# Optimization experiments

Measured on AMD Instinct MI355X. Metric: run time of the kernel, lower is better.

The kernel has to match this reference:

```python
import jax, jax.numpy as jnp
import numpy as np

NX = 65536   # spatial cells
T = 32       # time points
H = 128      # MLP hidden width
DX = 1.0     # spatial resolution (init kwarg dx)
S0, S1 = -1.0, 1.0  # fixed stencil (learn_stencil=False)


def setup_inputs() -> dict:
    key = jax.random.key(0)
    k1, k2, k3, k4 = jax.random.split(key, 4)
    t = jnp.arange(T, dtype=jnp.float32) * 0.01          # time grid, dt=0.01
    u0 = jax.random.uniform(k1, (NX,), jnp.float32)      # initial state
    inv_sqrt_h = jnp.float32(1.0 / np.sqrt(H))
    W1 = jax.random.normal(k2, (1, H), jnp.float32)
    W2 = jax.random.normal(k3, (H, H), jnp.float32) * inv_sqrt_h
    W3 = jax.random.normal(k4, (H, 1), jnp.float32) * inv_sqrt_h
    D = jnp.full((1,), 0.01, jnp.float32)                # diffusion coefficient
    BC = jnp.zeros((2, 1), jnp.float32)                  # Dirichlet BC values
    return {"t": t, "u0": u0, "W1": W1, "W2": W2, "W3": W3, "D": D, "BC": BC}


def _flux(u, W1, W2, W3, D, BC):
    # per-cell MLP (func_nn): Linear->Tanh->Linear->Tanh->Linear, no bias, no sigmoid
    h = jnp.tanh(u[:, None] @ W1)        # [Nx, H]
    h = jnp.tanh(h @ W2)                 # [Nx, H]
    a = (h @ W3)[:, 0]                   # [Nx]
    a_plus = jax.nn.relu(a)
    a_min = -jax.nn.relu(-a)
    d = D[0]
    # left fluxes
    lb = d * (S0 * u[0] + S1 * BC[0, 0]) - a_plus[0] / DX * (-S0 * u[0] - S1 * BC[0, 0])
    ln = d * (S0 * u[1:] + S1 * u[:-1]) - a_plus[1:] / DX * (-S0 * u[1:] - S1 * u[:-1])
    left = jnp.concatenate([lb[None], ln])
    # right fluxes
    rb = d * (S0 * u[-1] + S1 * BC[1, 0]) - a_min[-1] / DX * (S0 * u[-1] + S1 * BC[1, 0])
    rn = d * (S0 * u[:-1] + S1 * u[1:]) - a_min[:-1] / DX * (S0 * u[:-1] + S1 * u[1:])
    right = jnp.concatenate([rn, rb[None]])
    return left + right


def reference(t, u0, W1, W2, W3, D, BC):
    # Neural-ODE integration of du/dt = flux_kernel(u); fixed-step RK4 over grid t
    f = lambda u: _flux(u, W1, W2, W3, D, BC)

    def step(u, dt):
        k1 = f(u)
        k2 = f(u + 0.5 * dt * k1)
        k3 = f(u + 0.5 * dt * k2)
        k4 = f(u + dt * k3)
        un = u + (dt / 6.0) * (k1 + 2.0 * k2 + 2.0 * k3 + k4)
        return un, un

    _, us = jax.lax.scan(step, u0, jnp.diff(t))
    return jnp.concatenate([u0[None], us], axis=0)  # [T, Nx]
```

## Files before the change

### kernel.cpp

```cpp
#include <hip/hip_runtime.h>

#define NXC 65536
#define TT 32
#define HH 128
#define TABN 6145
#define TABNP 6146
#define TABLO (-1.0f)
#define TABINV 2048.0f
#define OUTW 32
#define VC 2
#define WINW 128
#define HALO 48

typedef __attribute__((ext_vector_type(8))) short bf16x8;
typedef __attribute__((ext_vector_type(4))) float f32x4;
typedef unsigned short u16;

__device__ __forceinline__ float bf2f(u16 b) {
    union { unsigned int u; float f; } v; v.u = ((unsigned int)b) << 16; return v.f;
}
__device__ __forceinline__ u16 f2bf(float f) {
    union { float f; unsigned int u; } v; v.f = f;
    return (u16)((v.u + 0x7fffu + ((v.u >> 16) & 1u)) >> 16);
}
__device__ __forceinline__ bool is_bf16_mode(const void* t) {
    return ((const u16*)t)[1] != 0;
}

#if __has_builtin(__builtin_amdgcn_exp2f)
#define EXP2F(x) __builtin_amdgcn_exp2f(x)
#else
#define EXP2F(x) exp2f(x)
#endif
#if __has_builtin(__builtin_amdgcn_rcpf)
#define RCPF(x) __builtin_amdgcn_rcpf(x)
#else
#define RCPF(x) (1.0f / (x))
#endif

__device__ __forceinline__ float fast_tanh(float x) {
    float e = EXP2F(x * 2.8853900817779268f);
    return 1.0f - 2.0f * RCPF(e + 1.0f);
}

__global__ void w2swz_kernel(const void* t, const void* W2,
                             u16* __restrict__ w2frag) {
    bool bf = is_bf16_mode(t);
    int i = blockIdx.x * 256 + threadIdx.x;
    int j = i & 7;
    int lane = (i >> 3) & 63;
    int ks = (i >> 9) & 3;
    int nt = i >> 11;
    int k = ks * 32 + (lane >> 4) * 8 + j;
    int n = nt * 16 + (lane & 15);
    w2frag[i] = bf ? ((const u16*)W2)[k * HH + n]
                   : f2bf(((const float*)W2)[k * HH + n]);
}

__global__ __launch_bounds__(256) void tabbuild_kernel(
    const void* traw, const void* W1, const void* W3,
    const u16* __restrict__ w2frag, float* __restrict__ atab) {
    __shared__ float w1s[HH];
    __shared__ float w3s[HH];
    bool bf = is_bf16_mode(traw);
    int tid = threadIdx.x;
    if (tid < HH)
        w1s[tid] = bf ? bf2f(((const u16*)W1)[tid]) : ((const float*)W1)[tid];
    else
        w3s[tid - HH] = bf ? bf2f(((const u16*)W3)[tid - HH])
                           : ((const float*)W3)[tid - HH];
    __syncthreads();

    int lane = tid & 63;
    int wave = tid >> 6;
    int q = lane >> 4;
    int m = lane & 15;
    int base = (blockIdx.x * 4 + wave) * 16;
    float uin = TABLO + (float)(base + m) * (1.0f / TABINV);

    bf16x8 afrag[4];
#pragma unroll
    for (int ks = 0; ks < 4; ++ks)
#pragma unroll
        for (int j = 0; j < 8; ++j) {
            float h = fast_tanh(uin * w1s[ks * 32 + q * 8 + j]);
            afrag[ks][j] = (short)f2bf(h);
        }

    const bf16x8* w2f = (const bf16x8*)w2frag;
    float p0 = 0.f, p1 = 0.f, p2 = 0.f, p3 = 0.f;
#pragma unroll
    for (int nt = 0; nt < 8; ++nt) {
        f32x4 acc = {0.f, 0.f, 0.f, 0.f};
#pragma unroll
        for (int ks = 0; ks < 4; ++ks) {
            bf16x8 b = w2f[(nt * 4 + ks) * 64 + lane];
            acc = __builtin_amdgcn_mfma_f32_16x16x32_bf16(afrag[ks], b, acc, 0, 0, 0);
        }
        float w3v = w3s[nt * 16 + m];
        p0 += fast_tanh(acc[0]) * w3v;
        p1 += fast_tanh(acc[1]) * w3v;
        p2 += fast_tanh(acc[2]) * w3v;
        p3 += fast_tanh(acc[3]) * w3v;
    }
#pragma unroll
    for (int sh = 1; sh < 16; sh <<= 1) {
        p0 += __shfl_xor(p0, sh, 64);
        p1 += __shfl_xor(p1, sh, 64);
        p2 += __shfl_xor(p2, sh, 64);
        p3 += __shfl_xor(p3, sh, 64);
    }
    int r = m & 3;
    float a = (r == 0) ? p0 : (r == 1) ? p1 : (r == 2) ? p2 : p3;
    if (m < 4) {
        int e = base + q * 4 + r;
        if (e < TABNP) atab[e] = a;
    }
}

__global__ void u0cvt_kernel(const void* t, const void* u0,
                             float* __restrict__ u, void* out) {
    bool bf = is_bf16_mode(t);
    int i = blockIdx.x * 256 + threadIdx.x;
    if (bf) {
        u16 v = ((const u16*)u0)[i];
        u[i] = bf2f(v);
        ((u16*)out)[i] = v;
    } else {
        float v = ((const float*)u0)[i];
        u[i] = v;
        ((float*)out)[i] = v;
    }
}

__global__ __launch_bounds__(256) void chunk_kernel(
    const void* traw, const float* __restrict__ uin, float* __restrict__ uout,
    const void* Draw, const void* BCraw, const float* __restrict__ atab,
    void* outbase, int s0, int nsteps) {
    __shared__ float2 tab[TABN];
    __shared__ float t32s[TT];

    int tid = threadIdx.x;
    bool bf = is_bf16_mode(traw);
    for (int i = tid; i < TABN; i += 256) {
        float v0 = atab[i];
        float v1 = atab[i + 1];
        tab[i] = make_float2(v0, v1 - v0);
    }
    if (tid < TT)
        t32s[tid] = bf ? bf2f(((const u16*)traw)[tid]) : ((const float*)traw)[tid];

    float d   = bf ? bf2f(((const u16*)Draw)[0])  : ((const float*)Draw)[0];
    float bc0 = bf ? bf2f(((const u16*)BCraw)[0]) : ((const float*)BCraw)[0];
    float bc1 = bf ? bf2f(((const u16*)BCraw)[1]) : ((const float*)BCraw)[1];

    int lane = tid & 63;
    int wid = blockIdx.x * 4 + (tid >> 6);
    int o0 = wid * OUTW;
    int wsg = o0 - HALO;
    int gb = wsg + lane * VC;
    int i0 = lane * VC;

    float v[VC], ub[VC], kacc[VC], kk[VC];
    bool gok[VC], isl[VC], isr[VC], own[VC];
#pragma unroll
    for (int j = 0; j < VC; ++j) {
        int g = gb + j;
        int i = i0 + j;
        gok[j] = (g >= 0) && (g < NXC);
        isl[j] = (g == 0);
        isr[j] = (g == NXC - 1);
        own[j] = (i >= HALO) && (i < HALO + OUTW);
        float x = gok[j] ? uin[g] : 0.f;
        v[j] = x;
        ub[j] = x;
    }
    __syncthreads();

    for (int st = 0; st < nsteps; ++st) {
        int step = s0 + st;
        float dt = t32s[step + 1] - t32s[step];
        float dt2 = 0.5f * dt, dt6 = dt * (1.0f / 6.0f);
#pragma unroll
        for (int j = 0; j < VC; ++j) kacc[j] = 0.f;
#pragma unroll
        for (int s = 0; s < 4; ++s) {
            int sigma = st * 4 + s;
            float cnext = (s < 2) ? dt2 : dt;
            float wgt = (s == 1 || s == 2) ? 2.f : 1.f;
            float vup = __shfl_up(v[VC - 1], 1, 64);
            float vdn = __shfl_down(v[0], 1, 64);
#pragma unroll
            for (int j = 0; j < VC; ++j) {
                float vc = v[j];
                float vl = (j == 0) ? vup : v[j - 1];
                float vr = (j == VC - 1) ? vdn : v[j + 1];
                vl = isl[j] ? bc0 : vl;
                vr = isr[j] ? bc1 : vr;
                float f = fmaf(vc, TABINV, (-TABLO) * TABINV);
                f = fminf(fmaxf(f, 0.0f), (float)(TABN - 1));
                int e0 = (int)f;
                float frac = f - (float)e0;
                float2 ts = tab[e0];
                float a = fmaf(frac, ts.y, ts.x);
                float ap = fmaxf(a, 0.f);
                float am = fminf(a, 0.f);
                float kv = (vl - vc) * (d + ap) + (vr - vc) * (d - am);
                int i = i0 + j;
                bool act = gok[j] && (i > sigma) && (i < WINW - 1 - sigma);
                kk[j] = act ? kv : 0.f;
            }
#pragma unroll
            for (int j = 0; j < VC; ++j) {
                int i = i0 + j;
                bool act = gok[j] && (i > sigma) && (i < WINW - 1 - sigma);
                kacc[j] += wgt * kk[j];
                if (act) {
                    if (s < 3) {
                        v[j] = fmaf(cnext, kk[j], ub[j]);
                    } else {
                        float vn = fmaf(dt6, kacc[j], ub[j]);
                        v[j] = vn;
                        ub[j] = vn;
                    }
                }
            }
        }
        size_t rb = (size_t)(step + 1) * NXC;
#pragma unroll
        for (int j = 0; j < VC; ++j) {
            if (own[j]) {
                if (bf) ((u16*)outbase)[rb + gb + j] = f2bf(ub[j]);
                else    ((float*)outbase)[rb + gb + j] = ub[j];
            }
        }
    }
#pragma unroll
    for (int j = 0; j < VC; ++j)
        if (own[j]) uout[gb + j] = ub[j];
}

extern "C" void kernel_launch(void* const* d_in, const int* in_sizes, int n_in,
                              void* d_out, int out_size, void* d_ws,
                              size_t ws_size, hipStream_t stream) {
    const void* t  = d_in[0];
    const void* u0 = d_in[1];
    const void* W1 = d_in[2];
    const void* W2 = d_in[3];
    const void* W3 = d_in[4];
    const void* Dp = d_in[5];
    const void* BC = d_in[6];

    float* atab = (float*)d_ws;
    u16* w2frag = (u16*)(atab + TABNP + 2);
    float* uA = (float*)(w2frag + 16384);
    float* uB = uA + NXC;

    w2swz_kernel<<<64, 256, 0, stream>>>(t, W2, w2frag);
    tabbuild_kernel<<<(TABNP + 63) / 64, 256, 0, stream>>>(t, W1, W3, w2frag, atab);
    u0cvt_kernel<<<NXC / 256, 256, 0, stream>>>(t, u0, uA, d_out);

    const int grid = NXC / (OUTW * 4);
    chunk_kernel<<<grid, 256, 0, stream>>>(t, uA, uB, Dp, BC, atab, d_out, 0, 12);
    chunk_kernel<<<grid, 256, 0, stream>>>(t, uB, uA, Dp, BC, atab, d_out, 12, 12);
    chunk_kernel<<<grid, 256, 0, stream>>>(t, uA, uB, Dp, BC, atab, d_out, 24, 7);
}
```

Measured before the change: 111.1 us.

## Shrink table range, fuse prep kernels, use one cell per lane with more chunks

Narrows the activation lookup table to the range [-0.5, 1.5], which shrinks the shared-memory table per block. The W2 swizzle moves into the table-build kernel through shared memory, and the u0 conversion moves into the first chunk kernel, removing two launches. Each lane now holds one cell instead of two, with smaller output windows and halos, and the time stepping is split into six chunk launches of about five steps instead of three. This trades more launches and more redundant halo recompute for less per-lane work and a cheaper table load per block. It also assumes the state stays inside the narrowed table range, and values outside are clamped.

Measured after the change: 131.4 us. +18.3%, slower.

```diff
diff --git a/kernel.cpp b/kernel.cpp
--- a/kernel.cpp
+++ b/kernel.cpp
@@ -3,14 +3,13 @@
 #define NXC 65536
 #define TT 32
 #define HH 128
-#define TABN 6145
-#define TABNP 6146
-#define TABLO (-1.0f)
+#define TABN 4097
+#define TABNP 4098
+#define TABLO (-0.5f)
 #define TABINV 2048.0f
-#define OUTW 32
-#define VC 2
-#define WINW 128
-#define HALO 48
+#define OUTW 16
+#define HALO 24
+#define GRID 1024
 
 typedef __attribute__((ext_vector_type(8))) short bf16x8;
 typedef __attribute__((ext_vector_type(4))) float f32x4;
@@ -43,25 +42,12 @@
     return 1.0f - 2.0f * RCPF(e + 1.0f);
 }
 
-__global__ void w2swz_kernel(const void* t, const void* W2,
-                             u16* __restrict__ w2frag) {
-    bool bf = is_bf16_mode(t);
-    int i = blockIdx.x * 256 + threadIdx.x;
-    int j = i & 7;
-    int lane = (i >> 3) & 63;
-    int ks = (i >> 9) & 3;
-    int nt = i >> 11;
-    int k = ks * 32 + (lane >> 4) * 8 + j;
-    int n = nt * 16 + (lane & 15);
-    w2frag[i] = bf ? ((const u16*)W2)[k * HH + n]
-                   : f2bf(((const float*)W2)[k * HH + n]);
-}
-
 __global__ __launch_bounds__(256) void tabbuild_kernel(
-    const void* traw, const void* W1, const void* W3,
-    const u16* __restrict__ w2frag, float* __restrict__ atab) {
+    const void* traw, const void* W1, const void* W2, const void* W3,
+    float* __restrict__ atab) {
     __shared__ float w1s[HH];
     __shared__ float w3s[HH];
+    __shared__ u16 w2s[HH * HH];
     bool bf = is_bf16_mode(traw);
     int tid = threadIdx.x;
     if (tid < HH)
@@ -69,6 +55,16 @@
     else
         w3s[tid - HH] = bf ? bf2f(((const u16*)W3)[tid - HH])
                            : ((const float*)W3)[tid - HH];
+#pragma unroll
+    for (int it = 0; it < 64; ++it) {
+        int idx = tid + it * 256;
+        u16 w = bf ? ((const u16*)W2)[idx] : f2bf(((const float*)W2)[idx]);
+        int k = idx >> 7, n = idx & 127;
+        int ks = k >> 5, hi = (k >> 3) & 3, j = k & 7;
+        int nt = n >> 4, lo = n & 15;
+        int lane = hi * 16 + lo;
+        w2s[((nt * 4 + ks) * 64 + lane) * 8 + j] = w;
+    }
     __syncthreads();
 
     int lane = tid & 63;
@@ -87,7 +83,7 @@
             afrag[ks][j] = (short)f2bf(h);
         }
 
-    const bf16x8* w2f = (const bf16x8*)w2frag;
+    const bf16x8* w2f = (const bf16x8*)w2s;
     float p0 = 0.f, p1 = 0.f, p2 = 0.f, p3 = 0.f;
 #pragma unroll
     for (int nt = 0; nt < 8; ++nt) {
@@ -118,23 +114,9 @@
     }
 }
 
-__global__ void u0cvt_kernel(const void* t, const void* u0,
-                             float* __restrict__ u, void* out) {
-    bool bf = is_bf16_mode(t);
-    int i = blockIdx.x * 256 + threadIdx.x;
-    if (bf) {
-        u16 v = ((const u16*)u0)[i];
-        u[i] = bf2f(v);
-        ((u16*)out)[i] = v;
-    } else {
-        float v = ((const float*)u0)[i];
-        u[i] = v;
-        ((float*)out)[i] = v;
-    }
-}
-
+template <int IS_FIRST>
 __global__ __launch_bounds__(256) void chunk_kernel(
-    const void* traw, const float* __restrict__ uin, float* __restrict__ uout,
+    const void* traw, const void* uinraw, float* __restrict__ uout,
     const void* Draw, const void* BCraw, const float* __restrict__ atab,
     void* outbase, int s0, int nsteps) {
     __shared__ float2 tab[TABN];
@@ -156,88 +138,63 @@
 
     int lane = tid & 63;
     int wid = blockIdx.x * 4 + (tid >> 6);
-    int o0 = wid * OUTW;
-    int wsg = o0 - HALO;
-    int gb = wsg + lane * VC;
-    int i0 = lane * VC;
-
-    float v[VC], ub[VC], kacc[VC], kk[VC];
-    bool gok[VC], isl[VC], isr[VC], own[VC];
-#pragma unroll
-    for (int j = 0; j < VC; ++j) {
-        int g = gb + j;
-        int i = i0 + j;
-        gok[j] = (g >= 0) && (g < NXC);
-        isl[j] = (g == 0);
-        isr[j] = (g == NXC - 1);
-        own[j] = (i >= HALO) && (i < HALO + OUTW);
-        float x = gok[j] ? uin[g] : 0.f;
-        v[j] = x;
-        ub[j] = x;
-    }
+    int g = wid * OUTW - HALO + lane;
+    bool gok = (g >= 0) && (g < NXC);
+    bool isl = (g == 0);
+    bool isr = (g == NXC - 1);
+    bool own = (lane >= HALO) && (lane < HALO + OUTW);
+
+    float x = 0.f;
+    if (IS_FIRST) {
+        if (gok)
+            x = bf ? bf2f(((const u16*)uinraw)[g]) : ((const float*)uinraw)[g];
+        if (own) {
+            if (bf) ((u16*)outbase)[g] = ((const u16*)uinraw)[g];
+            else    ((float*)outbase)[g] = x;
+        }
+    } else {
+        if (gok) x = ((const float*)uinraw)[g];
+    }
+    float v = x, ub = x;
     __syncthreads();
 
     for (int st = 0; st < nsteps; ++st) {
         int step = s0 + st;
         float dt = t32s[step + 1] - t32s[step];
         float dt2 = 0.5f * dt, dt6 = dt * (1.0f / 6.0f);
-#pragma unroll
-        for (int j = 0; j < VC; ++j) kacc[j] = 0.f;
+        float kacc = 0.f;
 #pragma unroll
         for (int s = 0; s < 4; ++s) {
             int sigma = st * 4 + s;
             float cnext = (s < 2) ? dt2 : dt;
             float wgt = (s == 1 || s == 2) ? 2.f : 1.f;
-            float vup = __shfl_up(v[VC - 1], 1, 64);
-            float vdn = __shfl_down(v[0], 1, 64);
-#pragma unroll
-            for (int j = 0; j < VC; ++j) {
-                float vc = v[j];
-                float vl = (j == 0) ? vup : v[j - 1];
-                float vr = (j == VC - 1) ? vdn : v[j + 1];
-                vl = isl[j] ? bc0 : vl;
-                vr = isr[j] ? bc1 : vr;
-                float f = fmaf(vc, TABINV, (-TABLO) * TABINV);
-                f = fminf(fmaxf(f, 0.0f), (float)(TABN - 1));
-                int e0 = (int)f;
-                float frac = f - (float)e0;
-                float2 ts = tab[e0];
-                float a = fmaf(frac, ts.y, ts.x);
-                float ap = fmaxf(a, 0.f);
-                float am = fminf(a, 0.f);
-                float kv = (vl - vc) * (d + ap) + (vr - vc) * (d - am);
-                int i = i0 + j;
-                bool act = gok[j] && (i > sigma) && (i < WINW - 1 - sigma);
-                kk[j] = act ? kv : 0.f;
+            float vup = __shfl_up(v, 1, 64);
+            float vdn = __shfl_down(v, 1, 64);
+            float vl = isl ? bc0 : vup;
+            float vr = isr ? bc1 : vdn;
+            float f = fmaf(v, TABINV, (-TABLO) * TABINV);
+            f = fminf(fmaxf(f, 0.0f), (float)(TABN - 1));
+            int e0 = (int)f;
+            float frac = f - (float)e0;
+            float2 ts = tab[e0];
+            float a = fmaf(frac, ts.y, ts.x);
+            float kv = (vl - v) * (d + fmaxf(a, 0.f)) +
+                       (vr - v) * (d - fminf(a, 0.f));
+            kacc = fmaf(wgt, kv, kacc);
+            bool act = gok && (lane > sigma) && (lane < 63 - sigma);
+            float vn = (s < 3) ? fmaf(cnext, kv, ub) : fmaf(dt6, kacc, ub);
+            if (act) {
+                v = vn;
+                if (s == 3) ub = vn;
             }
-#pragma unroll
-            for (int j = 0; j < VC; ++j) {
-                int i = i0 + j;
-                bool act = gok[j] && (i > sigma) && (i < WINW - 1 - sigma);
-                kacc[j] += wgt * kk[j];
-                if (act) {
-                    if (s < 3) {
-                        v[j] = fmaf(cnext, kk[j], ub[j]);
-                    } else {
-                        float vn = fmaf(dt6, kacc[j], ub[j]);
-                        v[j] = vn;
-                        ub[j] = vn;
-                    }
-                }
-            }
         }
         size_t rb = (size_t)(step + 1) * NXC;
-#pragma unroll
-        for (int j = 0; j < VC; ++j) {
-            if (own[j]) {
-                if (bf) ((u16*)outbase)[rb + gb + j] = f2bf(ub[j]);
-                else    ((float*)outbase)[rb + gb + j] = ub[j];
-            }
-        }
-    }
-#pragma unroll
-    for (int j = 0; j < VC; ++j)
-        if (own[j]) uout[gb + j] = ub[j];
+        if (own) {
+            if (bf) ((u16*)outbase)[rb + g] = f2bf(ub);
+            else    ((float*)outbase)[rb + g] = ub;
+        }
+    }
+    if (own) uout[g] = ub;
 }
 
 extern "C" void kernel_launch(void* const* d_in, const int* in_sizes, int n_in,
@@ -252,16 +209,15 @@
     const void* BC = d_in[6];
 
     float* atab = (float*)d_ws;
-    u16* w2frag = (u16*)(atab + TABNP + 2);
-    float* uA = (float*)(w2frag + 16384);
+    float* uA = atab + TABNP + 2;
     float* uB = uA + NXC;
 
-    w2swz_kernel<<<64, 256, 0, stream>>>(t, W2, w2frag);
-    tabbuild_kernel<<<(TABNP + 63) / 64, 256, 0, stream>>>(t, W1, W3, w2frag, atab);
-    u0cvt_kernel<<<NXC / 256, 256, 0, stream>>>(t, u0, uA, d_out);
-
-    const int grid = NXC / (OUTW * 4);
-    chunk_kernel<<<grid, 256, 0, stream>>>(t, uA, uB, Dp, BC, atab, d_out, 0, 12);
-    chunk_kernel<<<grid, 256, 0, stream>>>(t, uB, uA, Dp, BC, atab, d_out, 12, 12);
-    chunk_kernel<<<grid, 256, 0, stream>>>(t, uA, uB, Dp, BC, atab, d_out, 24, 7);
-}
+    tabbuild_kernel<<<(TABNP + 63) / 64, 256, 0, stream>>>(t, W1, W2, W3, atab);
+
+    chunk_kernel<1><<<GRID, 256, 0, stream>>>(t, u0, uB, Dp, BC, atab, d_out, 0, 6);
+    chunk_kernel<0><<<GRID, 256, 0, stream>>>(t, uB, uA, Dp, BC, atab, d_out, 6, 5);
+    chunk_kernel<0><<<GRID, 256, 0, stream>>>(t, uA, uB, Dp, BC, atab, d_out, 11, 5);
+    chunk_kernel<0><<<GRID, 256, 0, stream>>>(t, uB, uA, Dp, BC, atab, d_out, 16, 5);
+    chunk_kernel<0><<<GRID, 256, 0, stream>>>(t, uA, uB, Dp, BC, atab, d_out, 21, 5);
+    chunk_kernel<0><<<GRID, 256, 0, stream>>>(t, uB, uA, Dp, BC, atab, d_out, 26, 5);
+}
```
